# Kernel optimization log

Measured on AMD Instinct MI355X. Metric: run time of the kernel, lower is better.

The kernel has to match this reference:

```python
import jax, jax.numpy as jnp
import numpy as np

D_MODEL = 1024
NUM_HEADS = 16
D_HEAD = D_MODEL // NUM_HEADS


def setup_inputs() -> dict:
    key = jax.random.key(0)
    ks = jax.random.split(key, 11)
    B, S = 2, 2048
    s = 1.0 / np.sqrt(D_MODEL)
    inp = {
        "Q": jax.random.normal(ks[0], (B, S, D_MODEL), dtype=jnp.float32),
        "K": jax.random.normal(ks[1], (B, S, D_MODEL), dtype=jnp.float32),
        "V": jax.random.normal(ks[2], (B, S, D_MODEL), dtype=jnp.float32),
        "W_q": jax.random.normal(ks[3], (D_MODEL, D_MODEL), dtype=jnp.float32) * s,
        "b_q": jnp.zeros((D_MODEL,), dtype=jnp.float32),
        "W_k": jax.random.normal(ks[4], (D_MODEL, D_MODEL), dtype=jnp.float32) * s,
        "b_k": jnp.zeros((D_MODEL,), dtype=jnp.float32),
        "W_v": jax.random.normal(ks[5], (D_MODEL, D_MODEL), dtype=jnp.float32) * s,
        "b_v": jnp.zeros((D_MODEL,), dtype=jnp.float32),
        "W_o": jax.random.normal(ks[6], (D_MODEL, D_MODEL), dtype=jnp.float32) * s,
        "b_o": jnp.zeros((D_MODEL,), dtype=jnp.float32),
    }
    return inp


def reference(Q, K, V, W_q, b_q, W_k, b_k, W_v, b_v, W_o, b_o):
    B, S, _ = Q.shape
    # Linear projections (torch Linear: x @ W.T + b)
    q = Q @ W_q.T + b_q  # [B,S,D]
    k = K @ W_k.T + b_k
    v = V @ W_v.T + b_v
    # split heads -> [B,H,S,d]
    q = q.reshape(B, S, NUM_HEADS, D_HEAD).transpose(0, 2, 1, 3)
    k = k.reshape(B, S, NUM_HEADS, D_HEAD).transpose(0, 2, 1, 3)
    v = v.reshape(B, S, NUM_HEADS, D_HEAD).transpose(0, 2, 1, 3)
    scores = jnp.einsum("bhqd,bhkd->bhqk", q, k) / np.sqrt(D_HEAD).astype(np.float32)
    attn = jax.nn.softmax(scores, axis=-1)
    out = jnp.einsum("bhqk,bhkd->bhqd", attn, v)
    out = out.transpose(0, 2, 1, 3).reshape(B, S, D_MODEL)
    return out @ W_o.T + b_o
```

## Files before the change

kernel.cpp:

```cpp
#include <hip/hip_runtime.h>
#include <stdint.h>

#define D_MODEL 1024
#define S_LEN   2048
#define BATCH   2
#define NHEAD   16
#define DHEAD   64
#define NTOK    (BATCH * S_LEN)

typedef unsigned short u16;
typedef __attribute__((ext_vector_type(8))) short bf16x8;
typedef __attribute__((ext_vector_type(4))) float f32x4;
typedef __attribute__((ext_vector_type(16))) float f32x16;
typedef __attribute__((ext_vector_type(2))) unsigned int u32x2;

__device__ __forceinline__ unsigned pack2bf(float lo, float hi) {
    unsigned a = __float_as_uint(lo) + 0x8000u;
    unsigned b = __float_as_uint(hi) + 0x8000u;
    return __builtin_amdgcn_perm(b, a, 0x07060302u);
}
__device__ __forceinline__ u16 f2bf1(float f) {
    return (u16)((__float_as_uint(f) + 0x8000u) >> 16);
}

#define GAS(p) ((const __attribute__((address_space(1))) void*)(p))
#define LAS(p) ((__attribute__((address_space(3))) void*)(p))
#define SWZ8(row, c) (((((row) << 3) | ((c) ^ ((row) & 7)))) << 3)

__global__ __launch_bounds__(256) void convert_kernel(
    const float* __restrict__ Q, const float* __restrict__ K, const float* __restrict__ V,
    const float* __restrict__ Wq, const float* __restrict__ Wk,
    const float* __restrict__ Wv, const float* __restrict__ Wo,
    u16* __restrict__ Qb, u16* __restrict__ Kb, u16* __restrict__ Vb,
    u16* __restrict__ Wqb, u16* __restrict__ Wkb, u16* __restrict__ Wvb, u16* __restrict__ Wob)
{
    const size_t SEG = 262144;
    size_t start = (size_t)blockIdx.x * 4096;
    int s = (int)(start / SEG);
    const float* src; u16* dst; size_t seg0;
    if (s < 4)       { src = Q;  dst = Qb;  seg0 = 0; }
    else if (s < 8)  { src = K;  dst = Kb;  seg0 = 4 * SEG; }
    else if (s < 12) { src = V;  dst = Vb;  seg0 = 8 * SEG; }
    else if (s == 12){ src = Wq; dst = Wqb; seg0 = 12 * SEG; }
    else if (s == 13){ src = Wk; dst = Wkb; seg0 = 13 * SEG; }
    else if (s == 14){ src = Wv; dst = Wvb; seg0 = 14 * SEG; }
    else             { src = Wo; dst = Wob; seg0 = 15 * SEG; }
    size_t off = start - seg0 + threadIdx.x;
    const float4* s4 = (const float4*)src;
    #pragma unroll
    for (int k = 0; k < 16; ++k) {
        float4 x = s4[off + (size_t)k * 256];
        u32x2 p = (u32x2){pack2bf(x.x, x.y), pack2bf(x.z, x.w)};
        *(u32x2*)(dst + (off + (size_t)k * 256) * 4) = p;
    }
}

__global__ __launch_bounds__(512, 2) void proj_kernel(
    const u16* __restrict__ Qb, const u16* __restrict__ Kb, const u16* __restrict__ Vb,
    const u16* __restrict__ Wqb, const u16* __restrict__ Wkb, const u16* __restrict__ Wvb,
    const float* __restrict__ bq, const float* __restrict__ bk, const float* __restrict__ bv,
    u16* __restrict__ qw, u16* __restrict__ kw, u16* __restrict__ vtw)
{
    const int bid = blockIdx.x;
    const int wid = (bid & 7) * 24 + (bid >> 3);
    const int z = wid >> 6;
    const int r = wid & 63;
    const int nbase = (r >> 2) * 256;
    const int mbase = (r & 3) * 256;

    const u16* Ag = (z == 0) ? Wqb : (z == 1) ? Wkb : Wvb;
    const u16* Bg = (z == 0) ? Qb  : (z == 1) ? Kb  : Vb;
    const float* bias = (z == 0) ? bq : (z == 1) ? bk : bv;

    const int tid = threadIdx.x, lane = tid & 63, wave = tid >> 6;
    const int l31 = lane & 31, hh = lane >> 5;
    const int wm = wave >> 2;
    const int wn = wave & 3;

    __shared__ __align__(16) u16 smem[65536];

    size_t aoff[4], boff[4];
    #pragma unroll
    for (int c = 0; c < 4; ++c) {
        int p = (wave * 4 + c) * 64 + lane;
        int row = p >> 3;
        int cg  = (p & 7) ^ (row & 7);
        aoff[c] = (size_t)(mbase + row) * D_MODEL + cg * 8;
        boff[c] = (size_t)(nbase + row) * D_MODEL + cg * 8;
    }

#define STAGE(buf, kc)                                                              \
    do {                                                                            \
        _Pragma("unroll")                                                           \
        for (int c = 0; c < 4; ++c) {                                               \
            __builtin_amdgcn_global_load_lds(GAS(Ag + aoff[c] + (kc)),              \
                LAS(smem + (buf) * 16384 + (wave * 4 + c) * 512), 16, 0, 0);        \
            __builtin_amdgcn_global_load_lds(GAS(Bg + boff[c] + (kc)),              \
                LAS(smem + 32768 + (buf) * 16384 + (wave * 4 + c) * 512), 16, 0, 0);\
        }                                                                           \
    } while (0)

    STAGE(0, 0);

    f32x16 acc[4][2];
    #pragma unroll
    for (int mt = 0; mt < 4; ++mt)
        #pragma unroll
        for (int nt = 0; nt < 2; ++nt)
            #pragma unroll
            for (int q = 0; q < 16; ++q) acc[mt][nt][q] = 0.f;

    for (int t = 0; t < D_MODEL / 64; ++t) {
        const int cur = t & 1;
        asm volatile("s_waitcnt vmcnt(0) lgkmcnt(0)" ::: "memory");
        __builtin_amdgcn_s_barrier();
        asm volatile("" ::: "memory");
        if (t < D_MODEL / 64 - 1) STAGE(cur ^ 1, (t + 1) * 64);
        const u16* Ab = smem + cur * 16384;
        const u16* Bb = smem + 32768 + cur * 16384;
        #pragma unroll
        for (int kk = 0; kk < 4; ++kk) {
            bf16x8 af[4], bfr[2];
            #pragma unroll
            for (int mt = 0; mt < 4; ++mt)
                af[mt] = *(const bf16x8*)&Ab[SWZ8(wm * 128 + mt * 32 + l31, kk * 2 + hh)];
            #pragma unroll
            for (int nt = 0; nt < 2; ++nt)
                bfr[nt] = *(const bf16x8*)&Bb[SWZ8(wn * 64 + nt * 32 + l31, kk * 2 + hh)];
            #pragma unroll
            for (int mt = 0; mt < 4; ++mt)
                #pragma unroll
                for (int nt = 0; nt < 2; ++nt)
                    acc[mt][nt] = __builtin_amdgcn_mfma_f32_32x32x16_bf16(af[mt], bfr[nt], acc[mt][nt], 0, 0, 0);
        }
    }
#undef STAGE

    if (z < 2) {
        u16* Y = z ? kw : qw;
        const float scale = z ? 1.0f : 0.18033688011112042f;
        #pragma unroll
        for (int mt = 0; mt < 4; ++mt)
            #pragma unroll
            for (int nt = 0; nt < 2; ++nt) {
                const int tok = nbase + wn * 64 + nt * 32 + l31;
                u16* yrow = Y + (size_t)tok * D_MODEL;
                #pragma unroll
                for (int g = 0; g < 4; ++g) {
                    const int d0 = mbase + wm * 128 + mt * 32 + 8 * g + 4 * hh;
                    float4 b4 = *(const float4*)&bias[d0];
                    float v0 = (acc[mt][nt][4 * g + 0] + b4.x) * scale;
                    float v1 = (acc[mt][nt][4 * g + 1] + b4.y) * scale;
                    float v2 = (acc[mt][nt][4 * g + 2] + b4.z) * scale;
                    float v3 = (acc[mt][nt][4 * g + 3] + b4.w) * scale;
                    *(u32x2*)(yrow + d0) = (u32x2){pack2bf(v0, v1), pack2bf(v2, v3)};
                }
            }
    } else {
        #pragma unroll
        for (int mt = 0; mt < 4; ++mt)
            #pragma unroll
            for (int nt = 0; nt < 2; ++nt) {
                const int tok = nbase + wn * 64 + nt * 32 + l31;
                #pragma unroll
                for (int g = 0; g < 4; ++g) {
                    const int d0 = mbase + wm * 128 + mt * 32 + 8 * g + 4 * hh;
                    #pragma unroll
                    for (int q = 0; q < 4; ++q)
                        vtw[(size_t)(d0 + q) * NTOK + tok] =
                            f2bf1(acc[mt][nt][4 * g + q] + bias[d0 + q]);
                }
            }
    }
}

__global__ __launch_bounds__(512, 4) void attn_kernel(
    const u16* __restrict__ qw, const u16* __restrict__ kw,
    const u16* __restrict__ vtw, u16* __restrict__ aw)
{
    const int qbase = blockIdx.x * 128;
    const int h = blockIdx.y, b = blockIdx.z;
    const int tid = threadIdx.x, lane = tid & 63, wave = tid >> 6;
    const int wq = wave & 3;
    const int wk = wave >> 2;
    const int l31 = lane & 31;
    const int hh  = lane >> 5;
    const int colbase = h * DHEAD;
    const size_t qrow0 = (size_t)b * S_LEN + qbase;

    __shared__ __align__(16) u16 smem[17664];
    #define KS_OFF(buf) ((buf) * 4096)
    #define VS_OFF(buf) (8192 + (buf) * 4096)

    const int srow = tid >> 3;
    const int scg  = (tid & 7) ^ (srow & 7);
    const size_t ksrc = ((size_t)b * S_LEN + srow) * D_MODEL + colbase + scg * 8;
    const size_t vsrc = (size_t)(colbase + srow) * NTOK + (size_t)b * S_LEN + scg * 8;

    #define STAGE_KV(buf, kv0)                                                         \
        do {                                                                           \
            __builtin_amdgcn_global_load_lds(GAS(kw + ksrc + (size_t)(kv0) * D_MODEL), \
                                             LAS(smem + KS_OFF(buf) + wave * 512), 16, 0, 0); \
            __builtin_amdgcn_global_load_lds(GAS(vtw + vsrc + (kv0)),                  \
                                             LAS(smem + VS_OFF(buf) + wave * 512), 16, 0, 0); \
        } while (0)

    bf16x8 qf[4];
    {
        const u16* qptr = qw + (qrow0 + wq * 32 + l31) * D_MODEL + colbase + hh * 8;
        #pragma unroll
        for (int s = 0; s < 4; ++s) qf[s] = *(const bf16x8*)(qptr + s * 16);
    }

    STAGE_KV(0, 0);

    f32x16 o[2];
    #pragma unroll
    for (int dt = 0; dt < 2; ++dt)
        #pragma unroll
        for (int r = 0; r < 16; ++r) o[dt][r] = 0.f;
    float l = 0.f;

    __syncthreads();

    for (int t = 0; t < S_LEN / 64; ++t) {
        const int cur = t & 1;
        if (t + 1 < S_LEN / 64) STAGE_KV(!cur, (t + 1) * 64);

        f32x16 sc;
        #pragma unroll
        for (int r = 0; r < 16; ++r) sc[r] = -12.f;
        __builtin_amdgcn_s_setprio(1);
        #pragma unroll
        for (int s = 0; s < 4; ++s) {
            bf16x8 kf = *(const bf16x8*)&smem[KS_OFF(cur) + SWZ8(wk * 32 + l31, s * 2 + hh)];
            sc = __builtin_amdgcn_mfma_f32_32x32x16_bf16(kf, qf[s], sc, 0, 0, 0);
        }
        __builtin_amdgcn_s_setprio(0);

        unsigned x[4][2];
        #pragma unroll
        for (int g = 0; g < 4; ++g) {
            float p0 = __builtin_amdgcn_exp2f(sc[4 * g + 0]);
            float p1 = __builtin_amdgcn_exp2f(sc[4 * g + 1]);
            float p2 = __builtin_amdgcn_exp2f(sc[4 * g + 2]);
            float p3 = __builtin_amdgcn_exp2f(sc[4 * g + 3]);
            l += (p0 + p1) + (p2 + p3);
            asm("v_cvt_pk_bf16_f32 %0, %1, %2" : "=v"(x[g][0]) : "v"(p0), "v"(p1));
            asm("v_cvt_pk_bf16_f32 %0, %1, %2" : "=v"(x[g][1]) : "v"(p2), "v"(p3));
        }

        #pragma unroll
        for (int sp = 0; sp < 2; ++sp) {
            unsigned a0 = x[2 * sp][0], b0 = x[2 * sp + 1][0];
            unsigned a1 = x[2 * sp][1], b1 = x[2 * sp + 1][1];
            asm("v_permlane32_swap_b32 %0, %1" : "+v"(a0), "+v"(b0));
            asm("v_permlane32_swap_b32 %0, %1" : "+v"(a1), "+v"(b1));
            union { unsigned u[4]; bf16x8 v; } pf;
            pf.u[0] = a0; pf.u[1] = a1; pf.u[2] = b0; pf.u[3] = b1;
            __builtin_amdgcn_s_setprio(1);
            #pragma unroll
            for (int dt = 0; dt < 2; ++dt) {
                bf16x8 vf = *(const bf16x8*)&smem[VS_OFF(cur) + SWZ8(dt * 32 + l31, wk * 4 + sp * 2 + hh)];
                o[dt] = __builtin_amdgcn_mfma_f32_32x32x16_bf16(vf, pf.v, o[dt], 0, 0, 0);
            }
            __builtin_amdgcn_s_setprio(0);
        }

        __syncthreads();
    }

    l += __shfl_xor(l, 32);

    float* Ored = (float*)smem;
    float* Lred = (float*)(smem + 17408);
    float* op = Ored + ((size_t)wq * 32 + l31) * 68;
    if (wk == 1) {
        #pragma unroll
        for (int dt = 0; dt < 2; ++dt)
            #pragma unroll
            for (int g = 0; g < 4; ++g)
                *(f32x4*)(op + dt * 32 + 8 * g + 4 * hh) =
                    (f32x4){o[dt][4 * g + 0], o[dt][4 * g + 1], o[dt][4 * g + 2], o[dt][4 * g + 3]};
        if (hh == 0) Lred[wq * 32 + l31] = l;
    }
    __syncthreads();
    if (wk == 0) {
        l += Lred[wq * 32 + l31];
        float inv = 1.0f / l;
        size_t orow = (qrow0 + wq * 32 + l31) * D_MODEL + colbase;
        #pragma unroll
        for (int dt = 0; dt < 2; ++dt)
            #pragma unroll
            for (int g = 0; g < 4; ++g) {
                f32x4 add = *(const f32x4*)(op + dt * 32 + 8 * g + 4 * hh);
                float v0 = (o[dt][4 * g + 0] + add[0]) * inv;
                float v1 = (o[dt][4 * g + 1] + add[1]) * inv;
                float v2 = (o[dt][4 * g + 2] + add[2]) * inv;
                float v3 = (o[dt][4 * g + 3] + add[3]) * inv;
                *(u32x2*)(aw + orow + dt * 32 + 8 * g + 4 * hh) =
                    (u32x2){pack2bf(v0, v1), pack2bf(v2, v3)};
            }
    }
    #undef STAGE_KV
    #undef KS_OFF
    #undef VS_OFF
}

__global__ __launch_bounds__(512, 2) void outproj_kernel(
    const u16* __restrict__ aw, const u16* __restrict__ Wob,
    const float* __restrict__ bo, float* __restrict__ out)
{
    const int bid = blockIdx.x;
    const int wid = (bid & 7) * 32 + (bid >> 3);
    const int mbase = (wid & 7) * 128;
    const int nbase = (wid >> 3) * 128;

    const int tid = threadIdx.x, lane = tid & 63, wave = tid >> 6;
    const int l31 = lane & 31, hh = lane >> 5;
    const int wm = wave >> 2;
    const int wn = wave & 3;

    __shared__ __align__(16) u16 smem[32768];

    size_t aoff[2], boff[2];
    #pragma unroll
    for (int c = 0; c < 2; ++c) {
        int p = c * 512 + tid;
        int row = p >> 3;
        int cg  = (p & 7) ^ (row & 7);
        aoff[c] = (size_t)(mbase + row) * D_MODEL + cg * 8;
        boff[c] = (size_t)(nbase + row) * D_MODEL + cg * 8;
    }

#define OSTAGE(buf, kc)                                                             \
    do {                                                                            \
        _Pragma("unroll")                                                           \
        for (int c = 0; c < 2; ++c) {                                               \
            __builtin_amdgcn_global_load_lds(GAS(Wob + aoff[c] + (kc)),             \
                LAS(smem + (buf) * 8192 + c * 4096 + wave * 512), 16, 0, 0);        \
            __builtin_amdgcn_global_load_lds(GAS(aw + boff[c] + (kc)),              \
                LAS(smem + 16384 + (buf) * 8192 + c * 4096 + wave * 512), 16, 0, 0);\
        }                                                                           \
    } while (0)

    OSTAGE(0, 0);

    f32x16 acc[2];
    #pragma unroll
    for (int mt = 0; mt < 2; ++mt)
        #pragma unroll
        for (int q = 0; q < 16; ++q) acc[mt][q] = 0.f;

    for (int t = 0; t < D_MODEL / 64; ++t) {
        const int cur = t & 1;
        asm volatile("s_waitcnt vmcnt(0) lgkmcnt(0)" ::: "memory");
        __builtin_amdgcn_s_barrier();
        asm volatile("" ::: "memory");
        if (t < D_MODEL / 64 - 1) OSTAGE(cur ^ 1, (t + 1) * 64);
        const u16* Ab = smem + cur * 8192;
        const u16* Bb = smem + 16384 + cur * 8192;
        #pragma unroll
        for (int kk = 0; kk < 4; ++kk) {
            bf16x8 af[2], bfr;
            #pragma unroll
            for (int mt = 0; mt < 2; ++mt)
                af[mt] = *(const bf16x8*)&Ab[SWZ8(wm * 64 + mt * 32 + l31, kk * 2 + hh)];
            bfr = *(const bf16x8*)&Bb[SWZ8(wn * 32 + l31, kk * 2 + hh)];
            __builtin_amdgcn_s_setprio(1);
            #pragma unroll
            for (int mt = 0; mt < 2; ++mt)
                acc[mt] = __builtin_amdgcn_mfma_f32_32x32x16_bf16(af[mt], bfr, acc[mt], 0, 0, 0);
            __builtin_amdgcn_s_setprio(0);
        }
    }
#undef OSTAGE

    const int tok = nbase + wn * 32 + l31;
    float* orow = out + (size_t)tok * D_MODEL;
    #pragma unroll
    for (int mt = 0; mt < 2; ++mt)
        #pragma unroll
        for (int g = 0; g < 4; ++g) {
            const int d0 = mbase + wm * 64 + mt * 32 + 8 * g + 4 * hh;
            float4 b4 = *(const float4*)&bo[d0];
            float4 st;
            st.x = acc[mt][4 * g + 0] + b4.x;
            st.y = acc[mt][4 * g + 1] + b4.y;
            st.z = acc[mt][4 * g + 2] + b4.z;
            st.w = acc[mt][4 * g + 3] + b4.w;
            *(float4*)(orow + d0) = st;
        }
}

extern "C" void kernel_launch(void* const* d_in, const int* in_sizes, int n_in,
                              void* d_out, int out_size, void* d_ws, size_t ws_size,
                              hipStream_t stream) {
    const float* Q  = (const float*)d_in[0];
    const float* K  = (const float*)d_in[1];
    const float* V  = (const float*)d_in[2];
    const float* Wq = (const float*)d_in[3];
    const float* bq = (const float*)d_in[4];
    const float* Wk = (const float*)d_in[5];
    const float* bk = (const float*)d_in[6];
    const float* Wv = (const float*)d_in[7];
    const float* bv = (const float*)d_in[8];
    const float* Wo = (const float*)d_in[9];
    const float* bo = (const float*)d_in[10];

    const size_t NT = (size_t)NTOK * D_MODEL;
    const size_t WN = (size_t)D_MODEL * D_MODEL;
    u16* base = (u16*)d_ws;
    u16* qw  = base;
    u16* kw  = base + NT;
    u16* vtw = base + 2 * NT;
    u16* Qb  = base + 3 * NT;
    u16* Kb  = base + 4 * NT;
    u16* Vb  = base + 5 * NT;
    u16* Wqb = base + 6 * NT;
    u16* Wkb = Wqb + WN;
    u16* Wvb = Wkb + WN;
    u16* Wob = Wvb + WN;
    u16* aww = Qb;

    convert_kernel<<<1024, 256, 0, stream>>>(Q, K, V, Wq, Wk, Wv, Wo,
                                             Qb, Kb, Vb, Wqb, Wkb, Wvb, Wob);
    proj_kernel<<<dim3(192), 512, 0, stream>>>(Qb, Kb, Vb, Wqb, Wkb, Wvb,
                                               bq, bk, bv, qw, kw, vtw);
    attn_kernel<<<dim3(S_LEN / 128, NHEAD, BATCH), 512, 0, stream>>>(qw, kw, vtw, aww);
    outproj_kernel<<<dim3(256), 512, 0, stream>>>(aww, Wob, bo, (float*)d_out);
}
```

Before: 212.3 us.

## Double attention query tile per block and remap grid for XCD locality

Measured after the change: 210.6 us, median of 2. No clear change (-0.8%).

```diff
diff --git a/kernel.cpp b/kernel.cpp
--- a/kernel.cpp
+++ b/kernel.cpp
@@ -174,12 +174,16 @@
     }
 }
 
-__global__ __launch_bounds__(512, 4) void attn_kernel(
+__global__ __launch_bounds__(512, 2) void attn_kernel(
     const u16* __restrict__ qw, const u16* __restrict__ kw,
     const u16* __restrict__ vtw, u16* __restrict__ aw)
 {
-    const int qbase = blockIdx.x * 128;
-    const int h = blockIdx.y, b = blockIdx.z;
+    const int bid = blockIdx.x;
+    const int w = (bid & 7) * 32 + (bid >> 3);
+    const int qbase = (w & 7) * 256;
+    const int g = w >> 3;
+    const int h = g & 15, b = g >> 4;
+
     const int tid = threadIdx.x, lane = tid & 63, wave = tid >> 6;
     const int wq = wave & 3;
     const int wk = wave >> 2;
@@ -188,7 +192,7 @@
     const int colbase = h * DHEAD;
     const size_t qrow0 = (size_t)b * S_LEN + qbase;
 
-    __shared__ __align__(16) u16 smem[17664];
+    __shared__ __align__(16) u16 smem[35328];
     #define KS_OFF(buf) ((buf) * 4096)
     #define VS_OFF(buf) (8192 + (buf) * 4096)
 
@@ -205,21 +209,25 @@
                                              LAS(smem + VS_OFF(buf) + wave * 512), 16, 0, 0); \
         } while (0)
 
-    bf16x8 qf[4];
+    bf16x8 qf0[4], qf1[4];
     {
-        const u16* qptr = qw + (qrow0 + wq * 32 + l31) * D_MODEL + colbase + hh * 8;
-        #pragma unroll
-        for (int s = 0; s < 4; ++s) qf[s] = *(const bf16x8*)(qptr + s * 16);
+        const u16* qp0 = qw + (qrow0 + wq * 64 + l31) * D_MODEL + colbase + hh * 8;
+        const u16* qp1 = qw + (qrow0 + wq * 64 + 32 + l31) * D_MODEL + colbase + hh * 8;
+        #pragma unroll
+        for (int s = 0; s < 4; ++s) {
+            qf0[s] = *(const bf16x8*)(qp0 + s * 16);
+            qf1[s] = *(const bf16x8*)(qp1 + s * 16);
+        }
     }
 
     STAGE_KV(0, 0);
 
-    f32x16 o[2];
+    f32x16 o0[2], o1[2];
     #pragma unroll
     for (int dt = 0; dt < 2; ++dt)
         #pragma unroll
-        for (int r = 0; r < 16; ++r) o[dt][r] = 0.f;
-    float l = 0.f;
+        for (int r = 0; r < 16; ++r) { o0[dt][r] = 0.f; o1[dt][r] = 0.f; }
+    float l0 = 0.f, l1 = 0.f;
 
     __syncthreads();
 
@@ -227,42 +235,57 @@
         const int cur = t & 1;
         if (t + 1 < S_LEN / 64) STAGE_KV(!cur, (t + 1) * 64);
 
-        f32x16 sc;
-        #pragma unroll
-        for (int r = 0; r < 16; ++r) sc[r] = -12.f;
+        f32x16 sc0, sc1;
+        #pragma unroll
+        for (int r = 0; r < 16; ++r) { sc0[r] = -12.f; sc1[r] = -12.f; }
         __builtin_amdgcn_s_setprio(1);
         #pragma unroll
         for (int s = 0; s < 4; ++s) {
             bf16x8 kf = *(const bf16x8*)&smem[KS_OFF(cur) + SWZ8(wk * 32 + l31, s * 2 + hh)];
-            sc = __builtin_amdgcn_mfma_f32_32x32x16_bf16(kf, qf[s], sc, 0, 0, 0);
+            sc0 = __builtin_amdgcn_mfma_f32_32x32x16_bf16(kf, qf0[s], sc0, 0, 0, 0);
+            sc1 = __builtin_amdgcn_mfma_f32_32x32x16_bf16(kf, qf1[s], sc1, 0, 0, 0);
         }
         __builtin_amdgcn_s_setprio(0);
 
-        unsigned x[4][2];
-        #pragma unroll
-        for (int g = 0; g < 4; ++g) {
-            float p0 = __builtin_amdgcn_exp2f(sc[4 * g + 0]);
-            float p1 = __builtin_amdgcn_exp2f(sc[4 * g + 1]);
-            float p2 = __builtin_amdgcn_exp2f(sc[4 * g + 2]);
-            float p3 = __builtin_amdgcn_exp2f(sc[4 * g + 3]);
-            l += (p0 + p1) + (p2 + p3);
-            asm("v_cvt_pk_bf16_f32 %0, %1, %2" : "=v"(x[g][0]) : "v"(p0), "v"(p1));
-            asm("v_cvt_pk_bf16_f32 %0, %1, %2" : "=v"(x[g][1]) : "v"(p2), "v"(p3));
+        unsigned x0[4][2], x1[4][2];
+        #pragma unroll
+        for (int gg = 0; gg < 4; ++gg) {
+            float p0 = __builtin_amdgcn_exp2f(sc0[4 * gg + 0]);
+            float p1 = __builtin_amdgcn_exp2f(sc0[4 * gg + 1]);
+            float p2 = __builtin_amdgcn_exp2f(sc0[4 * gg + 2]);
+            float p3 = __builtin_amdgcn_exp2f(sc0[4 * gg + 3]);
+            l0 += (p0 + p1) + (p2 + p3);
+            asm("v_cvt_pk_bf16_f32 %0, %1, %2" : "=v"(x0[gg][0]) : "v"(p0), "v"(p1));
+            asm("v_cvt_pk_bf16_f32 %0, %1, %2" : "=v"(x0[gg][1]) : "v"(p2), "v"(p3));
+            float q0 = __builtin_amdgcn_exp2f(sc1[4 * gg + 0]);
+            float q1 = __builtin_amdgcn_exp2f(sc1[4 * gg + 1]);
+            float q2 = __builtin_amdgcn_exp2f(sc1[4 * gg + 2]);
+            float q3 = __builtin_amdgcn_exp2f(sc1[4 * gg + 3]);
+            l1 += (q0 + q1) + (q2 + q3);
+            asm("v_cvt_pk_bf16_f32 %0, %1, %2" : "=v"(x1[gg][0]) : "v"(q0), "v"(q1));
+            asm("v_cvt_pk_bf16_f32 %0, %1, %2" : "=v"(x1[gg][1]) : "v"(q2), "v"(q3));
         }
 
         #pragma unroll
         for (int sp = 0; sp < 2; ++sp) {
-            unsigned a0 = x[2 * sp][0], b0 = x[2 * sp + 1][0];
-            unsigned a1 = x[2 * sp][1], b1 = x[2 * sp + 1][1];
+            unsigned a0 = x0[2 * sp][0], b0 = x0[2 * sp + 1][0];
+            unsigned a1 = x0[2 * sp][1], b1 = x0[2 * sp + 1][1];
             asm("v_permlane32_swap_b32 %0, %1" : "+v"(a0), "+v"(b0));
             asm("v_permlane32_swap_b32 %0, %1" : "+v"(a1), "+v"(b1));
-            union { unsigned u[4]; bf16x8 v; } pf;
-            pf.u[0] = a0; pf.u[1] = a1; pf.u[2] = b0; pf.u[3] = b1;
+            union { unsigned u[4]; bf16x8 v; } pf0;
+            pf0.u[0] = a0; pf0.u[1] = a1; pf0.u[2] = b0; pf0.u[3] = b1;
+            unsigned c0 = x1[2 * sp][0], d0 = x1[2 * sp + 1][0];
+            unsigned c1 = x1[2 * sp][1], d1 = x1[2 * sp + 1][1];
+            asm("v_permlane32_swap_b32 %0, %1" : "+v"(c0), "+v"(d0));
+            asm("v_permlane32_swap_b32 %0, %1" : "+v"(c1), "+v"(d1));
+            union { unsigned u[4]; bf16x8 v; } pf1;
+            pf1.u[0] = c0; pf1.u[1] = c1; pf1.u[2] = d0; pf1.u[3] = d1;
             __builtin_amdgcn_s_setprio(1);
             #pragma unroll
             for (int dt = 0; dt < 2; ++dt) {
                 bf16x8 vf = *(const bf16x8*)&smem[VS_OFF(cur) + SWZ8(dt * 32 + l31, wk * 4 + sp * 2 + hh)];
-                o[dt] = __builtin_amdgcn_mfma_f32_32x32x16_bf16(vf, pf.v, o[dt], 0, 0, 0);
+                o0[dt] = __builtin_amdgcn_mfma_f32_32x32x16_bf16(vf, pf0.v, o0[dt], 0, 0, 0);
+                o1[dt] = __builtin_amdgcn_mfma_f32_32x32x16_bf16(vf, pf1.v, o1[dt], 0, 0, 0);
             }
             __builtin_amdgcn_s_setprio(0);
         }
@@ -270,36 +293,53 @@
         __syncthreads();
     }
 
-    l += __shfl_xor(l, 32);
+    l0 += __shfl_xor(l0, 32);
+    l1 += __shfl_xor(l1, 32);
 
     float* Ored = (float*)smem;
-    float* Lred = (float*)(smem + 17408);
-    float* op = Ored + ((size_t)wq * 32 + l31) * 68;
+    float* Lred = (float*)(smem + 34816);
+    float* op0 = Ored + ((size_t)wq * 64 + l31) * 68;
+    float* op1 = Ored + ((size_t)wq * 64 + 32 + l31) * 68;
     if (wk == 1) {
         #pragma unroll
         for (int dt = 0; dt < 2; ++dt)
             #pragma unroll
-            for (int g = 0; g < 4; ++g)
-                *(f32x4*)(op + dt * 32 + 8 * g + 4 * hh) =
-                    (f32x4){o[dt][4 * g + 0], o[dt][4 * g + 1], o[dt][4 * g + 2], o[dt][4 * g + 3]};
-        if (hh == 0) Lred[wq * 32 + l31] = l;
+            for (int gg = 0; gg < 4; ++gg) {
+                *(f32x4*)(op0 + dt * 32 + 8 * gg + 4 * hh) =
+                    (f32x4){o0[dt][4 * gg + 0], o0[dt][4 * gg + 1], o0[dt][4 * gg + 2], o0[dt][4 * gg + 3]};
+                *(f32x4*)(op1 + dt * 32 + 8 * gg + 4 * hh) =
+                    (f32x4){o1[dt][4 * gg + 0], o1[dt][4 * gg + 1], o1[dt][4 * gg + 2], o1[dt][4 * gg + 3]};
+            }
+        if (hh == 0) {
+            Lred[wq * 64 + l31] = l0;
+            Lred[wq * 64 + 32 + l31] = l1;
+        }
     }
     __syncthreads();
     if (wk == 0) {
-        l += Lred[wq * 32 + l31];
-        float inv = 1.0f / l;
-        size_t orow = (qrow0 + wq * 32 + l31) * D_MODEL + colbase;
+        l0 += Lred[wq * 64 + l31];
+        l1 += Lred[wq * 64 + 32 + l31];
+        float inv0 = 1.0f / l0, inv1 = 1.0f / l1;
+        size_t orow0 = (qrow0 + wq * 64 + l31) * D_MODEL + colbase;
+        size_t orow1 = (qrow0 + wq * 64 + 32 + l31) * D_MODEL + colbase;
         #pragma unroll
         for (int dt = 0; dt < 2; ++dt)
             #pragma unroll
-            for (int g = 0; g < 4; ++g) {
-                f32x4 add = *(const f32x4*)(op + dt * 32 + 8 * g + 4 * hh);
-                float v0 = (o[dt][4 * g + 0] + add[0]) * inv;
-                float v1 = (o[dt][4 * g + 1] + add[1]) * inv;
-                float v2 = (o[dt][4 * g + 2] + add[2]) * inv;
-                float v3 = (o[dt][4 * g + 3] + add[3]) * inv;
-                *(u32x2*)(aw + orow + dt * 32 + 8 * g + 4 * hh) =
+            for (int gg = 0; gg < 4; ++gg) {
+                f32x4 add0 = *(const f32x4*)(op0 + dt * 32 + 8 * gg + 4 * hh);
+                f32x4 add1 = *(const f32x4*)(op1 + dt * 32 + 8 * gg + 4 * hh);
+                float v0 = (o0[dt][4 * gg + 0] + add0[0]) * inv0;
+                float v1 = (o0[dt][4 * gg + 1] + add0[1]) * inv0;
+                float v2 = (o0[dt][4 * gg + 2] + add0[2]) * inv0;
+                float v3 = (o0[dt][4 * gg + 3] + add0[3]) * inv0;
+                *(u32x2*)(aw + orow0 + dt * 32 + 8 * gg + 4 * hh) =
                     (u32x2){pack2bf(v0, v1), pack2bf(v2, v3)};
+                float u0 = (o1[dt][4 * gg + 0] + add1[0]) * inv1;
+                float u1 = (o1[dt][4 * gg + 1] + add1[1]) * inv1;
+                float u2 = (o1[dt][4 * gg + 2] + add1[2]) * inv1;
+                float u3 = (o1[dt][4 * gg + 3] + add1[3]) * inv1;
+                *(u32x2*)(aw + orow1 + dt * 32 + 8 * gg + 4 * hh) =
+                    (u32x2){pack2bf(u0, u1), pack2bf(u2, u3)};
             }
     }
     #undef STAGE_KV
@@ -427,6 +467,6 @@
                                              Qb, Kb, Vb, Wqb, Wkb, Wvb, Wob);
     proj_kernel<<<dim3(192), 512, 0, stream>>>(Qb, Kb, Vb, Wqb, Wkb, Wvb,
                                                bq, bk, bv, qw, kw, vtw);
-    attn_kernel<<<dim3(S_LEN / 128, NHEAD, BATCH), 512, 0, stream>>>(qw, kw, vtw, aww);
+    attn_kernel<<<dim3(256), 512, 0, stream>>>(qw, kw, vtw, aww);
     outproj_kernel<<<dim3(256), 512, 0, stream>>>(aww, Wob, bo, (float*)d_out);
 }
```
